# Kernel tuning notes

Hardware: AMD Instinct MI355X
Metric: run time of the kernel (lower is better)

The kernel has to match this reference:

```python
import jax, jax.numpy as jnp
import numpy as np

R_MAX = 5.0
AVG_NEI = 16.0
NB = 8
L_OF_LM = np.repeat(np.arange(4), [1, 3, 5, 7])  # lm index -> l, 16 components for l_max=3


def real_sph(u):
    # real spherical harmonics up to l=3, component normalization; u: [E,3] unit vectors
    x, y, z = u[:, 0], u[:, 1], u[:, 2]
    x2, y2, z2 = x * x, y * y, z * z
    return jnp.stack([
        jnp.ones_like(x),
        1.7320508 * x, 1.7320508 * y, 1.7320508 * z,
        3.8729833 * x * y, 3.8729833 * y * z,
        1.1180340 * (3.0 * z2 - 1.0),
        3.8729833 * x * z, 1.9364917 * (x2 - y2),
        2.0916500 * y * (3.0 * x2 - y2), 10.246951 * x * y * z,
        1.6201852 * y * (5.0 * z2 - 1.0), 1.3228757 * z * (5.0 * z2 - 3.0),
        1.6201852 * x * (5.0 * z2 - 1.0), 5.1234753 * z * (x2 - y2),
        2.0916500 * x * (x2 - 3.0 * y2),
    ], axis=-1)


def radial_embed(r):
    # Bessel basis * polynomial (p=5) envelope, as in MACE RadialEmbeddingBlock
    n = jnp.arange(1, NB + 1, dtype=r.dtype)
    bess = jnp.sqrt(2.0 / R_MAX) * jnp.sin(n * jnp.pi * r[:, None] / R_MAX) / (r[:, None] + 1e-8)
    p = 5.0
    t = jnp.clip(r / R_MAX, 0.0, 1.0)
    env = 1.0 - 0.5 * (p + 1) * (p + 2) * t**p + p * (p + 2) * t**(p + 1) - 0.5 * p * (p + 1) * t**(p + 2)
    return bess * env[:, None]


def interaction(feats, Y, R, senders, receivers, Wu, Wd, num_nodes):
    # feats: [N,C,Din] (Din = sum of (2l+1) over input l-blocks); Y: [E,16]; R: [E,C,12] radial path weights
    n_lin = Wu.shape[0]
    up = jnp.concatenate([
        jnp.einsum('ncm,cd->ndm', feats[:, :, l * l:(l + 1) * (l + 1)], Wu[l])
        for l in range(n_lin)], axis=-1)
    hs = up[senders]  # gather sender features [E,C,Din]
    R0, R1, R2 = R[..., 0:4], R[..., 4:8], R[..., 8:12]
    # CG path (0, l_sh) -> l_sh : scalar feature times Y_l
    msg = R0[:, :, L_OF_LM] * hs[:, :, 0:1] * Y[:, None, :]  # [E,C,16]
    for l in range(1, n_lin):
        sl = slice(l * l, (l + 1) * (l + 1))
        # CG path (l, 0) -> l
        msg = msg.at[:, :, sl].add(R1[:, :, l:l + 1] * hs[:, :, sl] * Y[:, None, 0:1])
        # CG path (l, l) -> 0 : invariant dot product
        msg = msg.at[:, :, 0].add(R2[:, :, l] * jnp.sum(hs[:, :, sl] * Y[:, None, sl], axis=-1))
    agg = jnp.zeros((num_nodes, msg.shape[1], msg.shape[2]), msg.dtype).at[receivers].add(msg) / AVG_NEI
    return jnp.einsum('ncm,mcd->ndm', agg, Wd[L_OF_LM])  # per-l linear down


def setup_inputs() -> dict:
    key = jax.random.key(0)
    ks = jax.random.split(key, 18)
    N, E, C, S = 10000, 160000, 64, 10
    f32 = jnp.float32
    rn = lambda k, shape, scale: jax.random.normal(k, shape, f32) * scale
    return {
        'edge_vectors': rn(ks[0], (E, 3), 1.5),
        'node_embed': rn(ks[1], (S, C), 0.3),
        'rw1': rn(ks[2], (2, NB, 64), 1.0 / np.sqrt(NB)),
        'rw2': rn(ks[3], (2, 64, C * 12), 1.0 / np.sqrt(64)),
        'lu0': rn(ks[4], (1, C, C), 1.0 / np.sqrt(C)),
        'lu1': rn(ks[5], (2, C, C), 1.0 / np.sqrt(C)),
        'ld': rn(ks[6], (2, 4, C, C), 1.0 / np.sqrt(C)),
        'sel_w': rn(ks[7], (S, 4, C, C), 1.0 / np.sqrt(C)),
        'prod_w0': rn(ks[8], (S, C, C), 1.0 / np.sqrt(C)),
        'prod_w1': rn(ks[9], (S, C, C), 1.0 / np.sqrt(C)),
        'res_w': rn(ks[10], (S, C, C), 1.0 / np.sqrt(C)),
        'read0': rn(ks[11], (C, 1), 1.0 / np.sqrt(C)),
        'mlp_w1': rn(ks[12], (C, 32), 1.0 / np.sqrt(C)),
        'mlp_w2': rn(ks[13], (32, 1), 1.0 / np.sqrt(32)),
        'node_species': jax.random.randint(ks[14], (N,), 0, S),
        'senders': jax.random.randint(ks[15], (E,), 0, N),
        'receivers': jax.random.randint(ks[16], (E,), 0, N),
    }


def reference(edge_vectors, node_embed, rw1, rw2, lu0, lu1, ld, sel_w, prod_w0,
              prod_w1, res_w, read0, mlp_w1, mlp_w2, node_species, senders, receivers):
    N = node_species.shape[0]
    C = node_embed.shape[1]
    r = jnp.linalg.norm(edge_vectors, axis=-1)
    u = edge_vectors / (r[:, None] + 1e-8)
    Y = real_sph(u)                      # [E,16]
    rb = radial_embed(r)                 # [E,8]
    R_all = [(jax.nn.silu(rb @ rw1[i]) @ rw2[i]).reshape(-1, C, 12) for i in range(2)]
    # ---- layer 0 (selector_tp, not last) ----
    f = node_embed[node_species][:, :, None]               # [N,C,1] scalar embed
    f = interaction(f, Y, R_all[0], senders, receivers, lu0, ld[0], N)  # [N,C,16]
    blocks = []
    for l in range(4):  # species-dependent selector TP (per-l channel mixing)
        sl = slice(l * l, (l + 1) * (l + 1))
        blocks.append(jnp.einsum('ncm,ncd->ndm', f[:, :, sl], sel_w[node_species, l]))
    f = jnp.concatenate(blocks, axis=-1)
    # product basis (correlation 3 polynomial in invariant channel), target C x (0e+1o)
    s = f[:, :, 0]
    f1 = jnp.einsum('ncm,ncd->ndm', f[:, :, :4] * (1.0 + s + s * s)[:, :, None], prod_w0[node_species])
    out0 = f1[:, :, 0] @ read0           # linear readout head  [N,1]
    # ---- layer 1 (last, residual) ----
    res = jnp.einsum('nc,ncd->nd', f1[:, :, 0], res_w[node_species])
    g = interaction(f1, Y, R_all[1], senders, receivers, lu1, ld[1], N)  # [N,C,16]
    inv = g[:, :, 0] + jnp.sum(g[:, :, 1:] ** 2, axis=-1)  # invariants from all l blocks
    f2 = jnp.einsum('nc,ncd->nd', inv + inv * inv, prod_w1[node_species]) + res
    out1 = jax.nn.silu(f2 @ mlp_w1) @ mlp_w2  # nonlinear readout  [N,1]
    # stack heads (axis=2) then layers (axis=1): [N, num_interactions, num_heads, 1]
    return jnp.stack([out0, out1], axis=1)[:, :, None, :]
```

## Files before the change

kernel.cpp:

```cpp
#include <hip/hip_runtime.h>
#include <math.h>


typedef _Float16 half8 __attribute__((ext_vector_type(8)));
typedef float f32x4 __attribute__((ext_vector_type(4)));

__device__ __forceinline__ float silu_f(float x) { return x / (1.0f + expf(-x)); }

__device__ __forceinline__ float reduce64(float v) {
#pragma unroll
  for (int off = 32; off > 0; off >>= 1) v += __shfl_xor(v, off, 64);
  return v;
}

__device__ __forceinline__ void compute_Y(float x, float y, float z, float* Y) {
  float x2 = x * x, y2 = y * y, z2 = z * z;
  Y[0] = 1.0f;
  Y[1] = 1.7320508f * x;
  Y[2] = 1.7320508f * y;
  Y[3] = 1.7320508f * z;
  Y[4] = 3.8729833f * x * y;
  Y[5] = 3.8729833f * y * z;
  Y[6] = 1.118034f * (3.0f * z2 - 1.0f);
  Y[7] = 3.8729833f * x * z;
  Y[8] = 1.9364917f * (x2 - y2);
  Y[9] = 2.09165f * y * (3.0f * x2 - y2);
  Y[10] = 10.246951f * x * y * z;
  Y[11] = 1.6201852f * y * (5.0f * z2 - 1.0f);
  Y[12] = 1.3228757f * z * (5.0f * z2 - 3.0f);
  Y[13] = 1.6201852f * x * (5.0f * z2 - 1.0f);
  Y[14] = 5.1234753f * z * (x2 - y2);
  Y[15] = 2.09165f * x * (x2 - 3.0f * y2);
}

__device__ __forceinline__ void compute_rb(float r, float inv_r, float* rb) {
  float t = fminf(r * 0.2f, 1.0f);
  float t2 = t * t;
  float t5 = t2 * t2 * t;
  float env = 1.0f + t5 * (-21.0f + t * (35.0f - 15.0f * t));
  float th = 0.62831853f * r;
  float s1 = sinf(th), c1 = cosf(th);
  float c2 = 2.0f * c1;
  float sprev = 0.0f, scur = s1;
  float coef = 0.63245553f * inv_r * env;
#pragma unroll
  for (int k = 0; k < 8; k++) {
    rb[k] = coef * scur;
    float snxt = c2 * scur - sprev;
    sprev = scur; scur = snxt;
  }
}

__global__ __launch_bounds__(256) void k_hist(const int* __restrict__ receivers,
                                              int* __restrict__ cnt, int E) {
  int e = blockIdx.x * 256 + threadIdx.x;
  if (e < E) atomicAdd(&cnt[receivers[e]], 1);
}

__global__ __launch_bounds__(256) void k_scan(const int* __restrict__ deg,
                                              int* __restrict__ row_start,
                                              int* __restrict__ cursor, int N) {
  __shared__ int part[256];
  int t = threadIdx.x;
  int K = (N + 255) / 256;
  int lo = t * K, hi = min(lo + K, N);
  int s = 0;
  for (int i = lo; i < hi; i++) s += deg[i];
  part[t] = s;
  __syncthreads();
  for (int d = 1; d < 256; d <<= 1) {
    int v = (t >= d) ? part[t - d] : 0;
    __syncthreads();
    part[t] += v;
    __syncthreads();
  }
  int run = (t == 0) ? 0 : part[t - 1];
  for (int i = lo; i < hi; i++) {
    int di = deg[i];
    row_start[i] = run;
    cursor[i] = run;
    run += di;
  }
  if (t == 255) row_start[N] = part[255];
}

__global__ __launch_bounds__(256) void k_scatter(const int* __restrict__ receivers,
                                                 const int* __restrict__ senders,
                                                 int* __restrict__ cursor,
                                                 int* __restrict__ perm,
                                                 int* __restrict__ rsort,
                                                 int* __restrict__ ssort, int E) {
  int e = blockIdx.x * 256 + threadIdx.x;
  if (e < E) {
    int r = receivers[e];
    int pos = atomicAdd(&cursor[r], 1);
    perm[pos] = e;
    rsort[pos] = r;
    ssort[pos] = senders[e];
  }
}

__global__ __launch_bounds__(256) void k_pack(const float* __restrict__ rw2,
                                              _Float16* __restrict__ b1t,
                                              _Float16* __restrict__ b2t) {
  int idx = blockIdx.x * 256 + threadIdx.x;
  if (idx < 16384) {
    int n = idx >> 6, k = idx & 63;
    int c = n >> 2, j = n & 3;
    b1t[idx] = (_Float16)rw2[k * 768 + c * 12 + j];
  } else if (idx < 40960) {
    int i2 = idx - 16384;
    int n = i2 >> 6, k = i2 & 63;
    int c = n / 6, j = n - c * 6;
    int col = (j < 4) ? j : ((j == 4) ? 5 : 9);
    b2t[i2] = (_Float16)rw2[49152 + k * 768 + c * 12 + col];
  }
}

__global__ __launch_bounds__(256) void k_up0(const float* __restrict__ embed,
                                             const float* __restrict__ lu0,
                                             const int* __restrict__ species,
                                             float* __restrict__ up0, int N) {
  int wave = threadIdx.x >> 6, lane = threadIdx.x & 63;
  int n = (blockIdx.x << 2) + wave;
  if (n >= N) return;
  int sp = species[n];
  const float* er = embed + sp * 64;
  float acc = 0.0f;
#pragma unroll 8
  for (int c = 0; c < 64; c++) acc += er[c] * lu0[c * 64 + lane];
  up0[(size_t)n * 64 + lane] = acc;
}

__global__ __launch_bounds__(256) void k_geom(const float* __restrict__ ev,
                                              const float* __restrict__ rw1,
                                              const int* __restrict__ perm,
                                              _Float16* __restrict__ hid0,
                                              _Float16* __restrict__ hid1,
                                              float* __restrict__ Ysort,
                                              int* __restrict__ rsort,
                                              int* __restrict__ ssort,
                                              int E, int EPAD) {
  int wave = threadIdx.x >> 6, lane = threadIdx.x & 63;
  int j = blockIdx.x * 4 + wave;
  if (j >= EPAD) return;
  if (j >= E) {
    hid0[(size_t)j * 64 + lane] = (_Float16)0.0f;
    hid1[(size_t)j * 64 + lane] = (_Float16)0.0f;
    if (lane == 0) { rsort[j] = -1; ssort[j] = 0; }
    if (lane < 16) Ysort[(size_t)j * 16 + lane] = 0.0f;
    return;
  }
  int e = perm[j];
  float vx = ev[e * 3 + 0], vy = ev[e * 3 + 1], vz = ev[e * 3 + 2];
  float r = sqrtf(vx * vx + vy * vy + vz * vz);
  float inv_r = 1.0f / (r + 1e-8f);
  float Y[16]; compute_Y(vx * inv_r, vy * inv_r, vz * inv_r, Y);
  float rb[8]; compute_rb(r, inv_r, rb);

  float h0 = 0.0f, h1 = 0.0f;
#pragma unroll
  for (int k = 0; k < 8; k++) {
    h0 += rb[k] * rw1[k * 64 + lane];
    h1 += rb[k] * rw1[512 + k * 64 + lane];
  }
  hid0[(size_t)j * 64 + lane] = (_Float16)silu_f(h0);
  hid1[(size_t)j * 64 + lane] = (_Float16)silu_f(h1);

  float yv = Y[0];
#pragma unroll
  for (int m = 1; m < 16; m++) yv = (lane == m) ? Y[m] : yv;
  if (lane < 16) Ysort[(size_t)j * 16 + lane] = yv;
}

__global__ __launch_bounds__(256) void k_fagg1(const _Float16* __restrict__ hid,
                                               const _Float16* __restrict__ bt,
                                               const float* __restrict__ Ysort,
                                               const float* __restrict__ up0,
                                               const int* __restrict__ ssort,
                                               const int* __restrict__ rsort,
                                               float* __restrict__ agg, int E) {
  __shared__ _Float16 __attribute__((aligned(16))) lds[4][16 * 256];
  int wave = threadIdx.x >> 6, lane = threadIdx.x & 63;
  int q = lane >> 4, mr = lane & 15;
  _Float16* L = lds[wave];
  int j0 = __builtin_amdgcn_readfirstlane((blockIdx.x * 4 + wave) * 16);

  int rs[16], ss[16];
#pragma unroll
  for (int t = 0; t < 16; t++) {
    rs[t] = rsort[j0 + t];
    ss[t] = ssort[j0 + t];
  }
  float hsv[16];
#pragma unroll
  for (int t = 0; t < 16; t++)
    hsv[t] = up0[((size_t)ss[t] << 6) + lane];

  const half8* Ap = (const half8*)(hid + (size_t)(j0 + mr) * 64 + q * 8);
  half8 a0 = Ap[0];
  half8 a1 = Ap[4];
  const _Float16* bp = bt + (size_t)mr * 64 + q * 8;
#pragma unroll
  for (int T = 0; T < 16; T++) {
    half8 b0 = *(const half8*)(bp + T * 1024);
    half8 b1 = *(const half8*)(bp + T * 1024 + 32);
    f32x4 acc = {0.f, 0.f, 0.f, 0.f};
    acc = __builtin_amdgcn_mfma_f32_16x16x32_f16(a0, b0, acc, 0, 0, 0);
    acc = __builtin_amdgcn_mfma_f32_16x16x32_f16(a1, b1, acc, 0, 0, 0);
#pragma unroll
    for (int r = 0; r < 4; r++)
      L[(q * 4 + r) * 256 + T * 16 + mr] = (_Float16)acc[r];
  }

  float accm[16];
#pragma unroll
  for (int m = 0; m < 16; m++) accm[m] = 0.0f;
  int cur_r = (j0 < E) ? rs[0] : -1;

#pragma unroll
  for (int t = 0; t < 16; t++) {
    int j = j0 + t;
    bool ok = (j < E);
    int rr = ok ? rs[t] : -2;
    if (rr != cur_r) {
      if (cur_r >= 0) {
        float* base = agg + ((size_t)cur_r << 10) + lane;
#pragma unroll
        for (int m = 0; m < 16; m++) atomicAdd(base + (m << 6), accm[m]);
      }
#pragma unroll
      for (int m = 0; m < 16; m++) accm[m] = 0.0f;
      cur_r = rr;
    }
    if (ok) {
      float hs0 = hsv[t];
      const _Float16* Rr = L + t * 256 + lane * 4;
      float p0 = (float)Rr[0] * hs0, p1 = (float)Rr[1] * hs0;
      float p2 = (float)Rr[2] * hs0, p3 = (float)Rr[3] * hs0;
      const float* Yj = Ysort + (size_t)j * 16;
      float4 Ya = *(const float4*)(Yj);
      float4 Yb = *(const float4*)(Yj + 4);
      float4 Yc = *(const float4*)(Yj + 8);
      float4 Yd = *(const float4*)(Yj + 12);
      accm[0] += p0;
      accm[1] += p1 * Ya.y;  accm[2] += p1 * Ya.z;  accm[3] += p1 * Ya.w;
      accm[4] += p2 * Yb.x;  accm[5] += p2 * Yb.y;  accm[6] += p2 * Yb.z;
      accm[7] += p2 * Yb.w;  accm[8] += p2 * Yc.x;
      accm[9]  += p3 * Yc.y; accm[10] += p3 * Yc.z; accm[11] += p3 * Yc.w;
      accm[12] += p3 * Yd.x; accm[13] += p3 * Yd.y; accm[14] += p3 * Yd.z;
      accm[15] += p3 * Yd.w;
    }
  }
  if (cur_r >= 0) {
    float* base = agg + ((size_t)cur_r << 10) + lane;
#pragma unroll
    for (int m = 0; m < 16; m++) atomicAdd(base + (m << 6), accm[m]);
  }
}

__global__ __launch_bounds__(256) void k_fagg2(const _Float16* __restrict__ hid,
                                               const _Float16* __restrict__ bt,
                                               const float* __restrict__ Ysort,
                                               const float* __restrict__ up1,
                                               const int* __restrict__ ssort,
                                               const int* __restrict__ rsort,
                                               float* __restrict__ agg, int E) {
  __shared__ _Float16 __attribute__((aligned(16))) lds[4][16 * 384];
  int wave = threadIdx.x >> 6, lane = threadIdx.x & 63;
  int q = lane >> 4, mr = lane & 15;
  _Float16* L = lds[wave];
  int j0 = __builtin_amdgcn_readfirstlane((blockIdx.x * 4 + wave) * 16);

  int rs[16], ss[16];
#pragma unroll
  for (int t = 0; t < 16; t++) {
    rs[t] = rsort[j0 + t];
    ss[t] = ssort[j0 + t];
  }
  float4 hA[8];
#pragma unroll
  for (int t = 0; t < 8; t++)
    hA[t] = *(const float4*)(up1 + ((size_t)ss[t] << 8) + lane * 4);

  const half8* Ap = (const half8*)(hid + (size_t)(j0 + mr) * 64 + q * 8);
  half8 a0 = Ap[0];
  half8 a1 = Ap[4];
  const _Float16* bp = bt + (size_t)mr * 64 + q * 8;
#pragma unroll
  for (int T = 0; T < 24; T++) {
    half8 b0 = *(const half8*)(bp + T * 1024);
    half8 b1 = *(const half8*)(bp + T * 1024 + 32);
    f32x4 acc = {0.f, 0.f, 0.f, 0.f};
    acc = __builtin_amdgcn_mfma_f32_16x16x32_f16(a0, b0, acc, 0, 0, 0);
    acc = __builtin_amdgcn_mfma_f32_16x16x32_f16(a1, b1, acc, 0, 0, 0);
#pragma unroll
    for (int r = 0; r < 4; r++)
      L[(q * 4 + r) * 384 + T * 16 + mr] = (_Float16)acc[r];
  }

  float4 hB[8];
#pragma unroll
  for (int t = 0; t < 8; t++)
    hB[t] = *(const float4*)(up1 + ((size_t)ss[8 + t] << 8) + lane * 4);

  float accm[16];
#pragma unroll
  for (int m = 0; m < 16; m++) accm[m] = 0.0f;
  int cur_r = (j0 < E) ? rs[0] : -1;

#pragma unroll
  for (int t = 0; t < 16; t++) {
    int j = j0 + t;
    bool ok = (j < E);
    int rr = ok ? rs[t] : -2;
    if (rr != cur_r) {
      if (cur_r >= 0) {
        float* base = agg + ((size_t)cur_r << 10) + lane;
#pragma unroll
        for (int m = 0; m < 16; m++) atomicAdd(base + (m << 6), accm[m]);
      }
#pragma unroll
      for (int m = 0; m < 16; m++) accm[m] = 0.0f;
      cur_r = rr;
    }
    if (ok) {
      float4 hs = (t < 8) ? hA[t & 7] : hB[t & 7];
      float hs0 = hs.x, hs1 = hs.y, hs2 = hs.z, hs3 = hs.w;
      const _Float16* Rr = L + t * 384 + lane * 6;
      float R0 = (float)Rr[0], R1v = (float)Rr[1];
      float R2v = (float)Rr[2], R3v = (float)Rr[3];
      float c5 = (float)Rr[4], c9 = (float)Rr[5];
      float q0 = R0 * hs0, q1 = R1v * hs0, q2 = R2v * hs0, q3 = R3v * hs0;
      const float* Yj = Ysort + (size_t)j * 16;
      float4 Ya = *(const float4*)(Yj);
      float4 Yb = *(const float4*)(Yj + 4);
      float4 Yc = *(const float4*)(Yj + 8);
      float4 Yd = *(const float4*)(Yj + 12);
      accm[0] += q0 + c9 * (hs1 * Ya.y + hs2 * Ya.z + hs3 * Ya.w);
      accm[1] += q1 * Ya.y + c5 * hs1;
      accm[2] += q1 * Ya.z + c5 * hs2;
      accm[3] += q1 * Ya.w + c5 * hs3;
      accm[4] += q2 * Yb.x;  accm[5] += q2 * Yb.y;  accm[6] += q2 * Yb.z;
      accm[7] += q2 * Yb.w;  accm[8] += q2 * Yc.x;
      accm[9]  += q3 * Yc.y; accm[10] += q3 * Yc.z; accm[11] += q3 * Yc.w;
      accm[12] += q3 * Yd.x; accm[13] += q3 * Yd.y; accm[14] += q3 * Yd.z;
      accm[15] += q3 * Yd.w;
    }
  }
  if (cur_r >= 0) {
    float* base = agg + ((size_t)cur_r << 10) + lane;
#pragma unroll
    for (int m = 0; m < 16; m++) atomicAdd(base + (m << 6), accm[m]);
  }
}

__global__ __launch_bounds__(64) void k_node1(float* __restrict__ agg0,
                                              const float* __restrict__ ld0,
                                              const float* __restrict__ sel_w,
                                              const float* __restrict__ pw0,
                                              const float* __restrict__ res_w,
                                              const float* __restrict__ lu1,
                                              const float* __restrict__ read0,
                                              const int* __restrict__ species,
                                              float* __restrict__ out,
                                              float* __restrict__ res,
                                              float* __restrict__ up1, int N) {
  int n = blockIdx.x, d = threadIdx.x;
  int sp = species[n];
  __shared__ float sA[1024], sB[1024];

  float* ag = agg0 + ((size_t)n << 10);
#pragma unroll
  for (int m = 0; m < 16; m++) {
    sA[m * 64 + d] = ag[m * 64 + d] * 0.0625f;
    ag[m * 64 + d] = 0.0f;
  }
  __syncthreads();

  float fr[16];
#pragma unroll
  for (int m = 0; m < 16; m++) fr[m] = 0.0f;
#pragma unroll
  for (int l = 0; l < 4; l++) {
    int m0 = l * l, m1 = (l + 1) * (l + 1);
    const float* W = ld0 + l * 4096 + d;
#pragma unroll 8
    for (int c = 0; c < 64; c++) {
      float w = W[c * 64];
      for (int m = m0; m < m1; m++) fr[m] += sA[m * 64 + c] * w;
    }
  }
#pragma unroll
  for (int m = 0; m < 16; m++) sB[m * 64 + d] = fr[m];
  __syncthreads();

  float f2r[16];
#pragma unroll
  for (int m = 0; m < 16; m++) f2r[m] = 0.0f;
#pragma unroll
  for (int l = 0; l < 4; l++) {
    int m0 = l * l, m1 = (l + 1) * (l + 1);
    const float* W = sel_w + ((size_t)(sp * 4 + l) << 12) + d;
#pragma unroll 8
    for (int c = 0; c < 64; c++) {
      float w = W[c * 64];
      for (int m = m0; m < m1; m++) f2r[m] += sB[m * 64 + c] * w;
    }
  }
  float s0 = f2r[0];
  float tt = 1.0f + s0 + s0 * s0;
#pragma unroll
  for (int m = 0; m < 4; m++) sA[m * 64 + d] = f2r[m] * tt;
  __syncthreads();

  float f1r[4] = {0.f, 0.f, 0.f, 0.f};
  {
    const float* W = pw0 + ((size_t)sp << 12) + d;
#pragma unroll 8
    for (int c = 0; c < 64; c++) {
      float w = W[c * 64];
#pragma unroll
      for (int m = 0; m < 4; m++) f1r[m] += sA[m * 64 + c] * w;
    }
  }
#pragma unroll
  for (int m = 0; m < 4; m++) sB[m * 64 + d] = f1r[m];
  __syncthreads();

  float v = reduce64(f1r[0] * read0[d]);
  if (d == 0) out[2 * n] = v;

  float u0, u1v, u2v, u3v;
  {
    const float* Wr = res_w + ((size_t)sp << 12) + d;
    const float* Wu = lu1 + d;
    float a = 0.0f, b = 0.0f;
#pragma unroll 8
    for (int c = 0; c < 64; c++) {
      float fv = sB[c];
      a += fv * Wr[c * 64];
      b += fv * Wu[c * 64];
    }
    res[(size_t)n * 64 + d] = a;
    u0 = b;
  }
  {
    const float* Wu = lu1 + 4096 + d;
    float a1 = 0.f, a2 = 0.f, a3 = 0.f;
#pragma unroll 8
    for (int c = 0; c < 64; c++) {
      float w = Wu[c * 64];
      a1 += sB[64 + c] * w;
      a2 += sB[128 + c] * w;
      a3 += sB[192 + c] * w;
    }
    u1v = a1; u2v = a2; u3v = a3;
  }
  float4 uu = {u0, u1v, u2v, u3v};
  *(float4*)(up1 + ((size_t)n << 8) + d * 4) = uu;
}

__global__ __launch_bounds__(64) void k_node2(const float* __restrict__ agg1,
                                              const float* __restrict__ ld1,
                                              const float* __restrict__ pw1,
                                              const float* __restrict__ res,
                                              const float* __restrict__ mlp_w1,
                                              const float* __restrict__ mlp_w2,
                                              const int* __restrict__ species,
                                              float* __restrict__ out, int N) {
  int n = blockIdx.x, d = threadIdx.x;
  int sp = species[n];
  __shared__ float sA[1024];

  const float* ag = agg1 + ((size_t)n << 10);
#pragma unroll
  for (int m = 0; m < 16; m++) sA[m * 64 + d] = ag[m * 64 + d] * 0.0625f;
  __syncthreads();

  float g[16];
#pragma unroll
  for (int m = 0; m < 16; m++) g[m] = 0.0f;
#pragma unroll
  for (int l = 0; l < 4; l++) {
    int m0 = l * l, m1 = (l + 1) * (l + 1);
    const float* W = ld1 + l * 4096 + d;
#pragma unroll 8
    for (int c = 0; c < 64; c++) {
      float w = W[c * 64];
      for (int m = m0; m < m1; m++) g[m] += sA[m * 64 + c] * w;
    }
  }
  float inv = g[0];
#pragma unroll
  for (int m = 1; m < 16; m++) inv += g[m] * g[m];
  float qv = inv + inv * inv;
  __syncthreads();
  sA[d] = qv;
  __syncthreads();

  float a = res[(size_t)n * 64 + d];
  {
    const float* W = pw1 + ((size_t)sp << 12) + d;
#pragma unroll 8
    for (int c = 0; c < 64; c++) a += sA[c] * W[c * 64];
  }
  sA[64 + d] = a;
  __syncthreads();

  float val = 0.0f;
  if (d < 32) {
    float h = 0.0f;
#pragma unroll 8
    for (int c = 0; c < 64; c++) h += sA[64 + c] * mlp_w1[c * 32 + d];
    val = silu_f(h) * mlp_w2[d];
  }
  val = reduce64(val);
  if (d == 0) out[2 * n + 1] = val;
}

extern "C" void kernel_launch(void* const* d_in, const int* in_sizes, int n_in,
                              void* d_out, int out_size, void* d_ws, size_t ws_size,
                              hipStream_t stream) {
  const float* ev      = (const float*)d_in[0];
  const float* embed   = (const float*)d_in[1];
  const float* rw1     = (const float*)d_in[2];
  const float* rw2     = (const float*)d_in[3];
  const float* lu0     = (const float*)d_in[4];
  const float* lu1     = (const float*)d_in[5];
  const float* ld      = (const float*)d_in[6];
  const float* sel_w   = (const float*)d_in[7];
  const float* pw0     = (const float*)d_in[8];
  const float* pw1     = (const float*)d_in[9];
  const float* res_w   = (const float*)d_in[10];
  const float* read0   = (const float*)d_in[11];
  const float* mlp_w1  = (const float*)d_in[12];
  const float* mlp_w2  = (const float*)d_in[13];
  const int* species   = (const int*)d_in[14];
  const int* senders   = (const int*)d_in[15];
  const int* receivers = (const int*)d_in[16];
  float* out = (float*)d_out;

  int N = in_sizes[14];
  int E = in_sizes[15];
  int EPAD = ((E + 63) / 64) * 64;

  float* ws = (float*)d_ws;
  size_t o = 0;
  float* agg  = ws + o;  o += (size_t)N * 1024;
  float* up0  = ws + o;  o += (size_t)N * 64;
  float* up1  = ws + o;  o += (size_t)N * 256;
  float* resb = ws + o;  o += (size_t)N * 64;
  _Float16* b1t  = (_Float16*)(ws + o); o += 8192;
  _Float16* b2t  = (_Float16*)(ws + o); o += 12288;
  _Float16* hid0 = (_Float16*)(ws + o); o += (size_t)EPAD * 32;
  _Float16* hid1 = (_Float16*)(ws + o); o += (size_t)EPAD * 32;
  float* Ysort = ws + o; o += (size_t)EPAD * 16;
  int* row_start = (int*)(ws + o); o += (size_t)N + 1;
  int* cursor    = (int*)(ws + o); o += (size_t)N;
  int* perm      = (int*)(ws + o); o += (size_t)E;
  int* rsort     = (int*)(ws + o); o += (size_t)EPAD;
  int* ssort     = (int*)(ws + o); o += (size_t)EPAD;

  hipMemsetAsync(agg, 0, (size_t)N * 1024 * sizeof(float), stream);
  hipMemsetAsync(cursor, 0, (size_t)N * sizeof(int), stream);

  k_hist<<<(E + 255) / 256, 256, 0, stream>>>(receivers, cursor, E);
  k_scan<<<1, 256, 0, stream>>>(cursor, row_start, cursor, N);
  k_scatter<<<(E + 255) / 256, 256, 0, stream>>>(receivers, senders, cursor,
                                                 perm, rsort, ssort, E);

  k_pack<<<160, 256, 0, stream>>>(rw2, b1t, b2t);
  k_up0<<<(N + 3) / 4, 256, 0, stream>>>(embed, lu0, species, up0, N);
  k_geom<<<EPAD / 4, 256, 0, stream>>>(ev, rw1, perm, hid0, hid1, Ysort,
                                       rsort, ssort, E, EPAD);

  int fblocks = EPAD / 64;
  k_fagg1<<<fblocks, 256, 0, stream>>>(hid0, b1t, Ysort, up0, ssort, rsort, agg, E);
  k_node1<<<N, 64, 0, stream>>>(agg, ld, sel_w, pw0, res_w, lu1, read0, species,
                                out, resb, up1, N);
  k_fagg2<<<fblocks, 256, 0, stream>>>(hid1, b2t, Ysort, up1, ssort, rsort, agg, E);
  k_node2<<<N, 64, 0, stream>>>(agg, ld + 16384, pw1, resb, mlp_w1, mlp_w2, species, out, N);
}
```

Measured before the change: 500.0 us.

## Compute only l<=1 components in layer-0 aggregation and node update

Layer 0 only needs the 0e+1o components (the first four lm entries) downstream, because the product basis uses f[:, :, :4]. The first aggregation kernel now computes only two radial path columns per channel via MFMA, keeps four accumulators instead of sixteen, and atomically adds into a new compact N×256 buffer. k_node1 reads that compact buffer and does only the l=0 and l=1 channel mixing. This cuts MFMA work, LDS use, atomics and memory traffic in layer 0. In exchange a separate buffer is allocated and zeroed, and layer 1 no longer depends on node1 having cleared agg.

```diff
diff --git a/kernel.cpp b/kernel.cpp
--- a/kernel.cpp
+++ b/kernel.cpp
@@ -2,6 +2,8 @@
 #include <math.h>
 
 
+#define WAVE_SZ 64
+
 typedef _Float16 half8 __attribute__((ext_vector_type(8)));
 typedef float f32x4 __attribute__((ext_vector_type(4)));
 
@@ -9,7 +11,7 @@
 
 __device__ __forceinline__ float reduce64(float v) {
 #pragma unroll
-  for (int off = 32; off > 0; off >>= 1) v += __shfl_xor(v, off, 64);
+  for (int off = 32; off > 0; off >>= 1) v += __shfl_xor(v, off, WAVE_SZ);
   return v;
 }
 
@@ -47,7 +49,8 @@
   for (int k = 0; k < 8; k++) {
     rb[k] = coef * scur;
     float snxt = c2 * scur - sprev;
-    sprev = scur; scur = snxt;
+    sprev = scur;
+    scur = snxt;
   }
 }
 
@@ -104,12 +107,12 @@
                                               _Float16* __restrict__ b1t,
                                               _Float16* __restrict__ b2t) {
   int idx = blockIdx.x * 256 + threadIdx.x;
-  if (idx < 16384) {
+  if (idx < 8192) {
     int n = idx >> 6, k = idx & 63;
-    int c = n >> 2, j = n & 3;
+    int c = n >> 1, j = n & 1;
     b1t[idx] = (_Float16)rw2[k * 768 + c * 12 + j];
-  } else if (idx < 40960) {
-    int i2 = idx - 16384;
+  } else if (idx < 32768) {
+    int i2 = idx - 8192;
     int n = i2 >> 6, k = i2 & 63;
     int c = n / 6, j = n - c * 6;
     int col = (j < 4) ? j : ((j == 4) ? 5 : 9);
@@ -155,8 +158,10 @@
   float vx = ev[e * 3 + 0], vy = ev[e * 3 + 1], vz = ev[e * 3 + 2];
   float r = sqrtf(vx * vx + vy * vy + vz * vz);
   float inv_r = 1.0f / (r + 1e-8f);
-  float Y[16]; compute_Y(vx * inv_r, vy * inv_r, vz * inv_r, Y);
-  float rb[8]; compute_rb(r, inv_r, rb);
+  float Y[16];
+  compute_Y(vx * inv_r, vy * inv_r, vz * inv_r, Y);
+  float rb[8];
+  compute_rb(r, inv_r, rb);
 
   float h0 = 0.0f, h1 = 0.0f;
 #pragma unroll
@@ -179,8 +184,8 @@
                                                const float* __restrict__ up0,
                                                const int* __restrict__ ssort,
                                                const int* __restrict__ rsort,
-                                               float* __restrict__ agg, int E) {
-  __shared__ _Float16 __attribute__((aligned(16))) lds[4][16 * 256];
+                                               float* __restrict__ agg1c, int E) {
+  __shared__ _Float16 __attribute__((aligned(16))) lds[4][16 * 128];
   int wave = threadIdx.x >> 6, lane = threadIdx.x & 63;
   int q = lane >> 4, mr = lane & 15;
   _Float16* L = lds[wave];
@@ -194,15 +199,14 @@
   }
   float hsv[16];
 #pragma unroll
-  for (int t = 0; t < 16; t++)
-    hsv[t] = up0[((size_t)ss[t] << 6) + lane];
+  for (int t = 0; t < 16; t++) hsv[t] = up0[((size_t)ss[t] << 6) + lane];
 
   const half8* Ap = (const half8*)(hid + (size_t)(j0 + mr) * 64 + q * 8);
   half8 a0 = Ap[0];
   half8 a1 = Ap[4];
   const _Float16* bp = bt + (size_t)mr * 64 + q * 8;
 #pragma unroll
-  for (int T = 0; T < 16; T++) {
+  for (int T = 0; T < 8; T++) {
     half8 b0 = *(const half8*)(bp + T * 1024);
     half8 b1 = *(const half8*)(bp + T * 1024 + 32);
     f32x4 acc = {0.f, 0.f, 0.f, 0.f};
@@ -210,12 +214,10 @@
     acc = __builtin_amdgcn_mfma_f32_16x16x32_f16(a1, b1, acc, 0, 0, 0);
 #pragma unroll
     for (int r = 0; r < 4; r++)
-      L[(q * 4 + r) * 256 + T * 16 + mr] = (_Float16)acc[r];
-  }
-
-  float accm[16];
-#pragma unroll
-  for (int m = 0; m < 16; m++) accm[m] = 0.0f;
+      L[(q * 4 + r) * 128 + T * 16 + mr] = (_Float16)acc[r];
+  }
+
+  float accm[4] = {0.f, 0.f, 0.f, 0.f};
   int cur_r = (j0 < E) ? rs[0] : -1;
 
 #pragma unroll
@@ -225,37 +227,30 @@
     int rr = ok ? rs[t] : -2;
     if (rr != cur_r) {
       if (cur_r >= 0) {
-        float* base = agg + ((size_t)cur_r << 10) + lane;
-#pragma unroll
-        for (int m = 0; m < 16; m++) atomicAdd(base + (m << 6), accm[m]);
+        float* base = agg1c + ((size_t)cur_r << 8) + lane;
+#pragma unroll
+        for (int m = 0; m < 4; m++) atomicAdd(base + (m << 6), accm[m]);
       }
 #pragma unroll
-      for (int m = 0; m < 16; m++) accm[m] = 0.0f;
+      for (int m = 0; m < 4; m++) accm[m] = 0.0f;
       cur_r = rr;
     }
     if (ok) {
       float hs0 = hsv[t];
-      const _Float16* Rr = L + t * 256 + lane * 4;
-      float p0 = (float)Rr[0] * hs0, p1 = (float)Rr[1] * hs0;
-      float p2 = (float)Rr[2] * hs0, p3 = (float)Rr[3] * hs0;
-      const float* Yj = Ysort + (size_t)j * 16;
-      float4 Ya = *(const float4*)(Yj);
-      float4 Yb = *(const float4*)(Yj + 4);
-      float4 Yc = *(const float4*)(Yj + 8);
-      float4 Yd = *(const float4*)(Yj + 12);
+      const _Float16* Rr = L + t * 128 + lane * 2;
+      float p0 = (float)Rr[0] * hs0;
+      float p1 = (float)Rr[1] * hs0;
+      float4 Ya = *(const float4*)(Ysort + (size_t)j * 16);
       accm[0] += p0;
-      accm[1] += p1 * Ya.y;  accm[2] += p1 * Ya.z;  accm[3] += p1 * Ya.w;
-      accm[4] += p2 * Yb.x;  accm[5] += p2 * Yb.y;  accm[6] += p2 * Yb.z;
-      accm[7] += p2 * Yb.w;  accm[8] += p2 * Yc.x;
-      accm[9]  += p3 * Yc.y; accm[10] += p3 * Yc.z; accm[11] += p3 * Yc.w;
-      accm[12] += p3 * Yd.x; accm[13] += p3 * Yd.y; accm[14] += p3 * Yd.z;
-      accm[15] += p3 * Yd.w;
+      accm[1] += p1 * Ya.y;
+      accm[2] += p1 * Ya.z;
+      accm[3] += p1 * Ya.w;
     }
   }
   if (cur_r >= 0) {
-    float* base = agg + ((size_t)cur_r << 10) + lane;
-#pragma unroll
-    for (int m = 0; m < 16; m++) atomicAdd(base + (m << 6), accm[m]);
+    float* base = agg1c + ((size_t)cur_r << 8) + lane;
+#pragma unroll
+    for (int m = 0; m < 4; m++) atomicAdd(base + (m << 6), accm[m]);
   }
 }
 
@@ -341,10 +336,17 @@
       accm[1] += q1 * Ya.y + c5 * hs1;
       accm[2] += q1 * Ya.z + c5 * hs2;
       accm[3] += q1 * Ya.w + c5 * hs3;
-      accm[4] += q2 * Yb.x;  accm[5] += q2 * Yb.y;  accm[6] += q2 * Yb.z;
-      accm[7] += q2 * Yb.w;  accm[8] += q2 * Yc.x;
-      accm[9]  += q3 * Yc.y; accm[10] += q3 * Yc.z; accm[11] += q3 * Yc.w;
-      accm[12] += q3 * Yd.x; accm[13] += q3 * Yd.y; accm[14] += q3 * Yd.z;
+      accm[4] += q2 * Yb.x;
+      accm[5] += q2 * Yb.y;
+      accm[6] += q2 * Yb.z;
+      accm[7] += q2 * Yb.w;
+      accm[8] += q2 * Yc.x;
+      accm[9] += q3 * Yc.y;
+      accm[10] += q3 * Yc.z;
+      accm[11] += q3 * Yc.w;
+      accm[12] += q3 * Yd.x;
+      accm[13] += q3 * Yd.y;
+      accm[14] += q3 * Yd.z;
       accm[15] += q3 * Yd.w;
     }
   }
@@ -355,7 +357,7 @@
   }
 }
 
-__global__ __launch_bounds__(64) void k_node1(float* __restrict__ agg0,
+__global__ __launch_bounds__(64) void k_node1(const float* __restrict__ agg1c,
                                               const float* __restrict__ ld0,
                                               const float* __restrict__ sel_w,
                                               const float* __restrict__ pw0,
@@ -368,44 +370,41 @@
                                               float* __restrict__ up1, int N) {
   int n = blockIdx.x, d = threadIdx.x;
   int sp = species[n];
-  __shared__ float sA[1024], sB[1024];
-
-  float* ag = agg0 + ((size_t)n << 10);
-#pragma unroll
-  for (int m = 0; m < 16; m++) {
-    sA[m * 64 + d] = ag[m * 64 + d] * 0.0625f;
-    ag[m * 64 + d] = 0.0f;
-  }
-  __syncthreads();
-
-  float fr[16];
-#pragma unroll
-  for (int m = 0; m < 16; m++) fr[m] = 0.0f;
-#pragma unroll
-  for (int l = 0; l < 4; l++) {
-    int m0 = l * l, m1 = (l + 1) * (l + 1);
-    const float* W = ld0 + l * 4096 + d;
+  __shared__ float sA[256], sB[256];
+
+  const float* ag = agg1c + ((size_t)n << 8);
+#pragma unroll
+  for (int m = 0; m < 4; m++) sA[m * 64 + d] = ag[(m << 6) + d] * 0.0625f;
+  __syncthreads();
+
+  float fr[4] = {0.f, 0.f, 0.f, 0.f};
+  {
+    const float* W0 = ld0 + d;
+    const float* W1 = ld0 + 4096 + d;
 #pragma unroll 8
     for (int c = 0; c < 64; c++) {
-      float w = W[c * 64];
-      for (int m = m0; m < m1; m++) fr[m] += sA[m * 64 + c] * w;
-    }
-  }
-#pragma unroll
-  for (int m = 0; m < 16; m++) sB[m * 64 + d] = fr[m];
-  __syncthreads();
-
-  float f2r[16];
-#pragma unroll
-  for (int m = 0; m < 16; m++) f2r[m] = 0.0f;
-#pragma unroll
-  for (int l = 0; l < 4; l++) {
-    int m0 = l * l, m1 = (l + 1) * (l + 1);
-    const float* W = sel_w + ((size_t)(sp * 4 + l) << 12) + d;
+      float w0 = W0[c * 64], w1 = W1[c * 64];
+      fr[0] += sA[c] * w0;
+      fr[1] += sA[64 + c] * w1;
+      fr[2] += sA[128 + c] * w1;
+      fr[3] += sA[192 + c] * w1;
+    }
+  }
+#pragma unroll
+  for (int m = 0; m < 4; m++) sB[m * 64 + d] = fr[m];
+  __syncthreads();
+
+  float f2r[4] = {0.f, 0.f, 0.f, 0.f};
+  {
+    const float* W0 = sel_w + ((size_t)(sp * 4) << 12) + d;
+    const float* W1 = sel_w + ((size_t)(sp * 4 + 1) << 12) + d;
 #pragma unroll 8
     for (int c = 0; c < 64; c++) {
-      float w = W[c * 64];
-      for (int m = m0; m < m1; m++) f2r[m] += sB[m * 64 + c] * w;
+      float w0 = W0[c * 64], w1 = W1[c * 64];
+      f2r[0] += sB[c] * w0;
+      f2r[1] += sB[64 + c] * w1;
+      f2r[2] += sB[128 + c] * w1;
+      f2r[3] += sB[192 + c] * w1;
     }
   }
   float s0 = f2r[0];
@@ -431,7 +430,7 @@
   float v = reduce64(f1r[0] * read0[d]);
   if (d == 0) out[2 * n] = v;
 
-  float u0, u1v, u2v, u3v;
+  float u0;
   {
     const float* Wr = res_w + ((size_t)sp << 12) + d;
     const float* Wu = lu1 + d;
@@ -442,7 +441,7 @@
       a += fv * Wr[c * 64];
       b += fv * Wu[c * 64];
     }
-    res[(size_t)n * 64 + d] = a;
+    res[((size_t)n << 6) + d] = a;
     u0 = b;
   }
   {
@@ -455,10 +454,8 @@
       a2 += sB[128 + c] * w;
       a3 += sB[192 + c] * w;
     }
-    u1v = a1; u2v = a2; u3v = a3;
-  }
-  float4 uu = {u0, u1v, u2v, u3v};
-  *(float4*)(up1 + ((size_t)n << 8) + d * 4) = uu;
+    *(float4*)(up1 + ((size_t)n << 8) + d * 4) = make_float4(u0, a1, a2, a3);
+  }
 }
 
 __global__ __launch_bounds__(64) void k_node2(const float* __restrict__ agg1,
@@ -475,7 +472,7 @@
 
   const float* ag = agg1 + ((size_t)n << 10);
 #pragma unroll
-  for (int m = 0; m < 16; m++) sA[m * 64 + d] = ag[m * 64 + d] * 0.0625f;
+  for (int m = 0; m < 16; m++) sA[m * 64 + d] = ag[(m << 6) + d] * 0.0625f;
   __syncthreads();
 
   float g[16];
@@ -499,7 +496,7 @@
   sA[d] = qv;
   __syncthreads();
 
-  float a = res[(size_t)n * 64 + d];
+  float a = res[((size_t)n << 6) + d];
   {
     const float* W = pw1 + ((size_t)sp << 12) + d;
 #pragma unroll 8
@@ -547,22 +544,23 @@
 
   float* ws = (float*)d_ws;
   size_t o = 0;
-  float* agg  = ws + o;  o += (size_t)N * 1024;
-  float* up0  = ws + o;  o += (size_t)N * 64;
-  float* up1  = ws + o;  o += (size_t)N * 256;
-  float* resb = ws + o;  o += (size_t)N * 64;
-  _Float16* b1t  = (_Float16*)(ws + o); o += 8192;
+  float* agg   = ws + o;  o += (size_t)N * 1024;
+  float* agg1c = ws + o;  o += (size_t)N * 256;
+  float* up0   = ws + o;  o += (size_t)N * 64;
+  float* up1   = ws + o;  o += (size_t)N * 256;
+  float* resb  = ws + o;  o += (size_t)N * 64;
+  _Float16* b1t  = (_Float16*)(ws + o); o += 4096;
   _Float16* b2t  = (_Float16*)(ws + o); o += 12288;
   _Float16* hid0 = (_Float16*)(ws + o); o += (size_t)EPAD * 32;
   _Float16* hid1 = (_Float16*)(ws + o); o += (size_t)EPAD * 32;
-  float* Ysort = ws + o; o += (size_t)EPAD * 16;
+  float* Ysort = ws + o;  o += (size_t)EPAD * 16;
   int* row_start = (int*)(ws + o); o += (size_t)N + 1;
   int* cursor    = (int*)(ws + o); o += (size_t)N;
   int* perm      = (int*)(ws + o); o += (size_t)E;
   int* rsort     = (int*)(ws + o); o += (size_t)EPAD;
   int* ssort     = (int*)(ws + o); o += (size_t)EPAD;
 
-  hipMemsetAsync(agg, 0, (size_t)N * 1024 * sizeof(float), stream);
+  hipMemsetAsync(agg, 0, (size_t)N * 1280 * sizeof(float), stream);
   hipMemsetAsync(cursor, 0, (size_t)N * sizeof(int), stream);
 
   k_hist<<<(E + 255) / 256, 256, 0, stream>>>(receivers, cursor, E);
@@ -570,15 +568,18 @@
   k_scatter<<<(E + 255) / 256, 256, 0, stream>>>(receivers, senders, cursor,
                                                  perm, rsort, ssort, E);
 
-  k_pack<<<160, 256, 0, stream>>>(rw2, b1t, b2t);
+  k_pack<<<128, 256, 0, stream>>>(rw2, b1t, b2t);
   k_up0<<<(N + 3) / 4, 256, 0, stream>>>(embed, lu0, species, up0, N);
   k_geom<<<EPAD / 4, 256, 0, stream>>>(ev, rw1, perm, hid0, hid1, Ysort,
                                        rsort, ssort, E, EPAD);
 
   int fblocks = EPAD / 64;
-  k_fagg1<<<fblocks, 256, 0, stream>>>(hid0, b1t, Ysort, up0, ssort, rsort, agg, E);
-  k_node1<<<N, 64, 0, stream>>>(agg, ld, sel_w, pw0, res_w, lu1, read0, species,
-                                out, resb, up1, N);
-  k_fagg2<<<fblocks, 256, 0, stream>>>(hid1, b2t, Ysort, up1, ssort, rsort, agg, E);
-  k_node2<<<N, 64, 0, stream>>>(agg, ld + 16384, pw1, resb, mlp_w1, mlp_w2, species, out, N);
-}
+  k_fagg1<<<fblocks, 256, 0, stream>>>(hid0, b1t, Ysort, up0, ssort, rsort,
+                                       agg1c, E);
+  k_node1<<<N, 64, 0, stream>>>(agg1c, ld, sel_w, pw0, res_w, lu1, read0,
+                                species, out, resb, up1, N);
+  k_fagg2<<<fblocks, 256, 0, stream>>>(hid1, b2t, Ysort, up1, ssort, rsort,
+                                       agg, E);
+  k_node2<<<N, 64, 0, stream>>>(agg, ld + 16384, pw1, resb, mlp_w1, mlp_w2,
+                                species, out, N);
+}
```

Result: faster. 417.3 us (-16.5%).
